# Optimization experiments

Measured on AMD Instinct MI355X. Metric: run time of the kernel, lower is better.

The kernel has to match this reference:

```python
import jax, jax.numpy as jnp
import numpy as np

MAX_W, MIN_W = 120, 24


def setup_inputs() -> dict:
    key = jax.random.key(0)
    ks = jax.random.split(key, 11)
    B, S, D, H = 2, 2048, 1024, 16
    hd = D // H
    s = 1.0 / float(np.sqrt(D))
    return {
        "x": jax.random.normal(ks[0], (B, S, D), jnp.float32),
        "alpha": jnp.float32(0.1),
        "Wq": jax.random.normal(ks[1], (D, D), jnp.float32) * s,
        "bq": jnp.zeros((D,), jnp.float32),
        "Wk": jax.random.normal(ks[2], (D, D), jnp.float32) * s,
        "bk": jnp.zeros((D,), jnp.float32),
        "Wv": jax.random.normal(ks[3], (D, D), jnp.float32) * s,
        "bv": jnp.zeros((D,), jnp.float32),
        "W_o": jax.random.normal(ks[4], (H, hd, hd), jnp.float32),
        "Wfc": jax.random.normal(ks[5], (D, D), jnp.float32) * s,
        "bfc": jnp.zeros((D,), jnp.float32),
    }


def reference(x, alpha, Wq, bq, Wk, bk, Wv, bv, W_o, Wfc, bfc):
    B, S, D = x.shape
    H, hd, _ = W_o.shape
    # --- dynamic window size (step==0 path of the module) ---
    fluct = jnp.abs(x[:, -1] - x[:, -2])            # [B, D]
    a = jax.nn.sigmoid(alpha)
    ewma_prev = fluct[0, 0]                          # step==0: ewma_prev = fluct_step_value
    signal = a * fluct.mean() + (1.0 - a) * ewma_prev
    scale = jax.nn.sigmoid(signal)
    w = jnp.floor(MIN_W + (MAX_W - MIN_W) * scale).astype(jnp.int32)  # int() truncation
    half = w // 2
    # --- projections ---
    q = (x @ Wq + bq).reshape(B, S, H, hd).transpose(0, 2, 1, 3)  # [B,H,S,hd]
    k = (x @ Wk + bk).reshape(B, S, H, hd).transpose(0, 2, 1, 3)
    v = (x @ Wv + bv).reshape(B, S, H, hd).transpose(0, 2, 1, 3)
    inv_sqrt = 1.0 / float(np.sqrt(hd))
    scores = jnp.einsum('bhqd,bhkd->bhqk', q, k) * inv_sqrt       # [B,H,S,S]
    # banded window mask: allowed iff i - w//2 <= j <= i + w//2
    idx = jnp.arange(S)
    band = jnp.abs(idx[:, None] - idx[None, :]) <= half            # [S,S]
    scores = jnp.where(band[None, None], scores, -1e30)
    attn = jax.nn.softmax(scores, axis=-1)
    out = jnp.einsum('bhqk,bhkd->bhqd', attn, v)                   # [B,H,S,hd]
    out = jnp.einsum('bhqd,hdk->bhqk', out, W_o)                   # per-head output matmul
    out = out.transpose(0, 2, 1, 3).reshape(B, S, D)
    return out @ Wfc + bfc
```

## Files before the change

### kernel.cpp

```cpp
#include <hip/hip_runtime.h>
#include <hip/hip_bf16.h>
#include <stdint.h>
#include <stddef.h>

#define S_LEN 2048
#define DMODEL 1024
#define NHEAD 16
#define HDIM 64
#define BATCH 2
#define MROWS (BATCH * S_LEN)
#define QKV_LD 3072

typedef unsigned short u16;
typedef __attribute__((ext_vector_type(8))) short bf16x8;
typedef __attribute__((ext_vector_type(4))) float f32x4;

__device__ inline u16 f32_to_bf16(float f) {
  union { float f; unsigned int u; } v; v.f = f;
  unsigned int u = v.u;
  unsigned int r = (u + 0x7fffu + ((u >> 16) & 1u)) >> 16;
  return (u16)r;
}

__device__ inline void gload16(const u16* g, u16* l) {
  __builtin_amdgcn_global_load_lds(
      (const __attribute__((address_space(1))) unsigned int*)g,
      (__attribute__((address_space(3))) unsigned int*)l, 16, 0, 0);
}

__global__ __launch_bounds__(256) void prep(const float* __restrict__ x, u16* __restrict__ xb,
                                            const float* __restrict__ alpha, int* __restrict__ halfw,
                                            const float* __restrict__ Wq, const float* __restrict__ Wk,
                                            const float* __restrict__ Wv, u16* __restrict__ Wt) {
  __shared__ float lds[32 * 33];
  const int bid = blockIdx.x, tid = threadIdx.x;

  if (bid < 2048) {
    size_t i = ((size_t)bid * 256 + tid) * 8;
    float4 v0 = *(const float4*)(x + i);
    float4 v1 = *(const float4*)(x + i + 4);
    bf16x8 r;
    r[0] = (short)f32_to_bf16(v0.x); r[1] = (short)f32_to_bf16(v0.y);
    r[2] = (short)f32_to_bf16(v0.z); r[3] = (short)f32_to_bf16(v0.w);
    r[4] = (short)f32_to_bf16(v1.x); r[5] = (short)f32_to_bf16(v1.y);
    r[6] = (short)f32_to_bf16(v1.z); r[7] = (short)f32_to_bf16(v1.w);
    *(bf16x8*)(xb + i) = r;
  } else if (bid == 2048) {
    float s = 0.f;
    for (int i = tid; i < BATCH * DMODEL; i += 256) {
      int b = i >> 10, d = i & 1023;
      size_t base = (size_t)b * S_LEN * DMODEL + d;
      float f1 = x[base + (size_t)(S_LEN - 1) * DMODEL];
      float f0 = x[base + (size_t)(S_LEN - 2) * DMODEL];
      s += fabsf(f1 - f0);
    }
#pragma unroll
    for (int m = 32; m >= 1; m >>= 1) s += __shfl_xor(s, m, 64);
    if ((tid & 63) == 0) lds[tid >> 6] = s;
    __syncthreads();
    if (tid == 0) {
      float total = lds[0] + lds[1] + lds[2] + lds[3];
      float mean = total / (float)(BATCH * DMODEL);
      float e1 = x[(size_t)(S_LEN - 1) * DMODEL];
      float e0 = x[(size_t)(S_LEN - 2) * DMODEL];
      float ew = fabsf(e1 - e0);
      float a = 1.f / (1.f + expf(-alpha[0]));
      float sig = a * mean + (1.f - a) * ew;
      float scale = 1.f / (1.f + expf(-sig));
      int wv = (int)floorf(24.f + 96.f * scale);
      *halfw = wv >> 1;
    }
  } else {
    float (*tile)[33] = (float (*)[33])lds;
    const int r = bid - 2049;
    const int z = r >> 10, rem = r & 1023;
    const int k0 = (rem >> 5) * 32, n0 = (rem & 31) * 32;
    const float* W = z == 0 ? Wq : (z == 1 ? Wk : Wv);
    const int tx = tid & 31, ty = tid >> 5;
#pragma unroll
    for (int i = 0; i < 4; ++i)
      tile[ty + i * 8][tx] = W[(size_t)(k0 + ty + i * 8) * DMODEL + n0 + tx];
    __syncthreads();
    u16* o = Wt + (size_t)z * DMODEL * DMODEL;
#pragma unroll
    for (int i = 0; i < 4; ++i)
      o[(size_t)(n0 + ty + i * 8) * DMODEL + k0 + tx] = f32_to_bf16(tile[tx][ty + i * 8]);
  }
}

__global__ __launch_bounds__(128) void build_wc(const float* __restrict__ W_o,
                                                const float* __restrict__ Wfc,
                                                u16* __restrict__ Wc_t) {
  __shared__ float lds[64 * 128];
  int nb = blockIdx.x, h = blockIdx.y, tx = threadIdx.x;
  int n0 = nb * 128;
#pragma unroll
  for (int c = 0; c < 64; ++c)
    lds[c * 128 + tx] = Wfc[(size_t)(h * 64 + c) * DMODEL + n0 + tx];
  __syncthreads();
  float acc[64];
#pragma unroll
  for (int d = 0; d < 64; ++d) acc[d] = 0.f;
  for (int c = 0; c < 64; ++c) {
    float wv = lds[c * 128 + tx];
#pragma unroll
    for (int d = 0; d < 64; ++d)
      acc[d] += W_o[(size_t)(h * 64 + d) * 64 + c] * wv;
  }
  u16 tmp[64];
#pragma unroll
  for (int d = 0; d < 64; ++d) tmp[d] = f32_to_bf16(acc[d]);
  u16* dst = Wc_t + (size_t)(n0 + tx) * DMODEL + h * 64;
#pragma unroll
  for (int q = 0; q < 8; ++q)
    *(bf16x8*)(dst + q * 8) = *(bf16x8*)(tmp + q * 8);
}

__global__ __launch_bounds__(256, 2) void gemm_qkv(
    const u16* __restrict__ A, const u16* __restrict__ Bt,
    const float* __restrict__ bq, const float* __restrict__ bk,
    const float* __restrict__ bv, u16* __restrict__ out) {
  __shared__ __align__(16) u16 smem[2][256 * 64];

  const int tid = threadIdx.x;
  const int l = tid & 63, w = tid >> 6;
  const int wr = w >> 1, wc = w & 1;
  const int lrow = l & 15, lk = l >> 4;

  const int xcd = blockIdx.x & 7;
  const int idx = blockIdx.x >> 3;
  const int bm = idx & 31;
  const int bn = xcd * 3 + (idx >> 5);
  const int rowA0 = bm * 128;
  const int colB0 = bn * 128;

  f32x4 acc[4][4] = {};

  auto stage = [&](int buf, int kt) {
    u16* As = smem[buf];
    u16* Bs = smem[buf] + 128 * 64;
#pragma unroll
    for (int i = 0; i < 4; ++i) {
      int c = i * 256 + tid;
      int row = c >> 3, u = c & 7;
      const u16* g = A + (size_t)(rowA0 + row) * DMODEL + kt + ((u ^ (row & 7)) << 3);
      gload16(g, As + c * 8);
    }
#pragma unroll
    for (int i = 0; i < 4; ++i) {
      int c = i * 256 + tid;
      int row = c >> 3, u = c & 7;
      const u16* g = Bt + (size_t)(colB0 + row) * DMODEL + kt + ((u ^ (row & 7)) << 3);
      gload16(g, Bs + c * 8);
    }
  };

  stage(0, 0);

  int buf = 0;
#pragma unroll 1
  for (int t = 0; t < 16; ++t) {
    __builtin_amdgcn_s_barrier();
    if (t < 15) {
      stage(buf ^ 1, (t + 1) * 64);
      asm volatile("s_waitcnt vmcnt(8)" ::: "memory");
    } else {
      asm volatile("s_waitcnt vmcnt(0)" ::: "memory");
    }
    __builtin_amdgcn_s_barrier();
    asm volatile("" ::: "memory");

    const u16* As = smem[buf];
    const u16* Bs = smem[buf] + 128 * 64;
    __builtin_amdgcn_s_setprio(1);
#pragma unroll
    for (int kk = 0; kk < 2; ++kk) {
      const int swz = ((((kk << 2) + lk) ^ (lrow & 7)) << 3);
      bf16x8 af[4], bg[4];
#pragma unroll
      for (int m = 0; m < 4; ++m)
        af[m] = *(const bf16x8*)(As + (wr * 64 + m * 16 + lrow) * 64 + swz);
#pragma unroll
      for (int n = 0; n < 4; ++n)
        bg[n] = *(const bf16x8*)(Bs + (wc * 64 + n * 16 + lrow) * 64 + swz);
#pragma unroll
      for (int m = 0; m < 4; ++m)
#pragma unroll
        for (int n = 0; n < 4; ++n)
          acc[m][n] = __builtin_amdgcn_mfma_f32_16x16x32_bf16(af[m], bg[n], acc[m][n], 0, 0, 0);
    }
    __builtin_amdgcn_s_setprio(0);
    buf ^= 1;
  }

#pragma unroll
  for (int n = 0; n < 4; ++n) {
    int c = colB0 + wc * 64 + n * 16 + lrow;
    float bias = (c < 1024) ? bq[c] : ((c < 2048) ? bk[c - 1024] : bv[c - 2048]);
    float mult = (c < 1024) ? 0.125f : 1.0f;
#pragma unroll
    for (int m = 0; m < 4; ++m) {
      int r0 = rowA0 + wr * 64 + m * 16 + lk * 4;
#pragma unroll
      for (int j = 0; j < 4; ++j)
        out[(size_t)(r0 + j) * QKV_LD + c] = f32_to_bf16((acc[m][n][j] + bias) * mult);
    }
  }
}

__global__ __launch_bounds__(256, 2) void gemm_fc(const u16* __restrict__ A,
                                                  const u16* __restrict__ Bt,
                                                  const float* __restrict__ bias,
                                                  float* __restrict__ out) {
  __shared__ __align__(16) u16 smem[2][192 * 64];

  const int tid = threadIdx.x;
  const int l = tid & 63, w = tid >> 6;
  const int wr = w >> 1, wc = w & 1;
  const int lrow = l & 15, lk = l >> 4;

  const int bn = blockIdx.x & 7;
  const int bm = blockIdx.x >> 3;
  const int rowA0 = bm * 64, colB0 = bn * 128;

  f32x4 acc[2][4] = {};

  auto stage = [&](int buf, int kt) {
    u16* As = smem[buf];
    u16* Bs = smem[buf] + 64 * 64;
#pragma unroll
    for (int i = 0; i < 2; ++i) {
      int c = i * 256 + tid;
      int row = c >> 3, u = c & 7;
      const u16* g = A + (size_t)(rowA0 + row) * DMODEL + kt + ((u ^ (row & 7)) << 3);
      gload16(g, As + c * 8);
    }
#pragma unroll
    for (int i = 0; i < 4; ++i) {
      int c = i * 256 + tid;
      int row = c >> 3, u = c & 7;
      const u16* g = Bt + (size_t)(colB0 + row) * DMODEL + kt + ((u ^ (row & 7)) << 3);
      gload16(g, Bs + c * 8);
    }
  };

  stage(0, 0);

  int buf = 0;
#pragma unroll 1
  for (int t = 0; t < 16; ++t) {
    __builtin_amdgcn_s_barrier();
    if (t < 15) {
      stage(buf ^ 1, (t + 1) * 64);
      asm volatile("s_waitcnt vmcnt(6)" ::: "memory");
    } else {
      asm volatile("s_waitcnt vmcnt(0)" ::: "memory");
    }
    __builtin_amdgcn_s_barrier();
    asm volatile("" ::: "memory");

    const u16* As = smem[buf];
    const u16* Bs = smem[buf] + 64 * 64;
    __builtin_amdgcn_s_setprio(1);
#pragma unroll
    for (int kk = 0; kk < 2; ++kk) {
      const int swz = ((((kk << 2) + lk) ^ (lrow & 7)) << 3);
      bf16x8 af[2], bg[4];
#pragma unroll
      for (int m = 0; m < 2; ++m)
        af[m] = *(const bf16x8*)(As + (wr * 32 + m * 16 + lrow) * 64 + swz);
#pragma unroll
      for (int n = 0; n < 4; ++n)
        bg[n] = *(const bf16x8*)(Bs + (wc * 64 + n * 16 + lrow) * 64 + swz);
#pragma unroll
      for (int m = 0; m < 2; ++m)
#pragma unroll
        for (int n = 0; n < 4; ++n)
          acc[m][n] = __builtin_amdgcn_mfma_f32_16x16x32_bf16(af[m], bg[n], acc[m][n], 0, 0, 0);
    }
    __builtin_amdgcn_s_setprio(0);
    buf ^= 1;
  }

#pragma unroll
  for (int n = 0; n < 4; ++n) {
    int c = colB0 + wc * 64 + n * 16 + lrow;
    float bv = bias[c];
#pragma unroll
    for (int m = 0; m < 2; ++m) {
      int r0 = rowA0 + wr * 32 + m * 16 + lk * 4;
#pragma unroll
      for (int j = 0; j < 4; ++j)
        out[(size_t)(r0 + j) * DMODEL + c] = acc[m][n][j] + bv;
    }
  }
}

__global__ __launch_bounds__(256) void attn_win(const u16* __restrict__ qkv,
                                                u16* __restrict__ ao,
                                                const int* __restrict__ halfptr) {
  __shared__ __align__(16) u16 KP[12800];
  __shared__ __align__(16) u16 Vt[64 * 200];
  const int tid = threadIdx.x, l = tid & 63, w = tid >> 6;
  const int lrow = l & 15, lk = l >> 4;
  const int q0 = blockIdx.x * 64, k0 = q0 - 64;
  const int h = blockIdx.y, b = blockIdx.z;
  const int halfw = *halfptr;

  const u16* qb = qkv;
  const u16* kb = qkv + 1024;
  const u16* vb = qkv + 2048;

#pragma unroll
  for (int i = 0; i < 6; ++i) {
    int c = i * 256 + tid;
    int row = c >> 3, u = c & 7;
    const u16* g = kb + (ptrdiff_t)((b * S_LEN + k0 + row) * QKV_LD + h * 64 + ((u ^ (row & 7)) << 3));
    gload16(g, KP + c * 8);
  }
  const int qrow = q0 + w * 16 + lrow;
  bf16x8 qf[2];
#pragma unroll
  for (int kk = 0; kk < 2; ++kk)
    qf[kk] = *(const bf16x8*)(qb + (ptrdiff_t)((b * S_LEN + qrow) * QKV_LD + h * 64 + kk * 32 + lk * 8));
  bf16x8 vreg[6];
#pragma unroll
  for (int i = 0; i < 6; ++i) {
    int c = i * 256 + tid;
    int row = c % 192, ch = c / 192;
    vreg[i] = *(const bf16x8*)(vb + (ptrdiff_t)((b * S_LEN + k0 + row) * QKV_LD + h * 64 + ch * 8));
  }

  asm volatile("s_waitcnt vmcnt(0)" ::: "memory");
  __syncthreads();

  f32x4 sc[12];
#pragma unroll
  for (int f = 0; f < 12; ++f) sc[f] = (f32x4){0.f, 0.f, 0.f, 0.f};
#pragma unroll
  for (int kk = 0; kk < 2; ++kk) {
#pragma unroll
    for (int f = 0; f < 12; ++f) {
      bf16x8 kf = *(const bf16x8*)(KP + (f * 16 + lrow) * 64 + ((((kk << 2) + lk) ^ (lrow & 7)) << 3));
      sc[f] = __builtin_amdgcn_mfma_f32_16x16x32_bf16(qf[kk], kf, sc[f], 0, 0, 0);
    }
  }

#pragma unroll
  for (int i = 0; i < 6; ++i) {
    int c = i * 256 + tid;
    int row = c % 192, ch = c / 192;
#pragma unroll
    for (int e = 0; e < 8; ++e)
      Vt[(ch * 8 + e) * 200 + row] = (u16)vreg[i][e];
  }

  float rmax[4] = {-3e38f, -3e38f, -3e38f, -3e38f};
  const int qbase = q0 + w * 16 + lk * 4;
#pragma unroll
  for (int f = 0; f < 12; ++f) {
    int kj = k0 + f * 16 + lrow;
    bool kok = (kj >= 0) && (kj < S_LEN);
#pragma unroll
    for (int j = 0; j < 4; ++j) {
      int qi = qbase + j;
      float v = sc[f][j];
      int dd = qi - kj;
      int ad = dd < 0 ? -dd : dd;
      v = (kok && ad <= halfw) ? v : -1e30f;
      sc[f][j] = v;
      rmax[j] = fmaxf(rmax[j], v);
    }
  }
#pragma unroll
  for (int j = 0; j < 4; ++j) {
    rmax[j] = fmaxf(rmax[j], __shfl_xor(rmax[j], 1, 16));
    rmax[j] = fmaxf(rmax[j], __shfl_xor(rmax[j], 2, 16));
    rmax[j] = fmaxf(rmax[j], __shfl_xor(rmax[j], 4, 16));
    rmax[j] = fmaxf(rmax[j], __shfl_xor(rmax[j], 8, 16));
  }
  float rsum[4] = {0.f, 0.f, 0.f, 0.f};
#pragma unroll
  for (int f = 0; f < 12; ++f)
#pragma unroll
    for (int j = 0; j < 4; ++j) {
      float e = __expf(sc[f][j] - rmax[j]);
      sc[f][j] = e;
      rsum[j] += e;
    }
#pragma unroll
  for (int j = 0; j < 4; ++j) {
    rsum[j] += __shfl_xor(rsum[j], 1, 16);
    rsum[j] += __shfl_xor(rsum[j], 2, 16);
    rsum[j] += __shfl_xor(rsum[j], 4, 16);
    rsum[j] += __shfl_xor(rsum[j], 8, 16);
  }
  float rinv[4];
#pragma unroll
  for (int j = 0; j < 4; ++j) rinv[j] = 1.0f / rsum[j];

  __syncthreads();

  u16* Ps = KP;
#pragma unroll
  for (int f = 0; f < 12; ++f)
#pragma unroll
    for (int j = 0; j < 4; ++j) {
      int prow = w * 16 + lk * 4 + j;
      Ps[prow * 200 + f * 16 + lrow] = f32_to_bf16(sc[f][j] * rinv[j]);
    }
  __syncthreads();

  f32x4 o[4] = {};
#pragma unroll
  for (int jt = 0; jt < 6; ++jt) {
    bf16x8 pa = *(const bf16x8*)(Ps + (w * 16 + lrow) * 200 + jt * 32 + lk * 8);
#pragma unroll
    for (int n = 0; n < 4; ++n) {
      bf16x8 vf = *(const bf16x8*)(Vt + (n * 16 + lrow) * 200 + jt * 32 + lk * 8);
      o[n] = __builtin_amdgcn_mfma_f32_16x16x32_bf16(pa, vf, o[n], 0, 0, 0);
    }
  }
#pragma unroll
  for (int n = 0; n < 4; ++n)
#pragma unroll
    for (int j = 0; j < 4; ++j) {
      int qi = q0 + w * 16 + lk * 4 + j;
      int d = n * 16 + lrow;
      ao[(size_t)(b * S_LEN + qi) * DMODEL + h * 64 + d] = f32_to_bf16(o[n][j]);
    }
}

extern "C" void kernel_launch(void* const* d_in, const int* in_sizes, int n_in,
                              void* d_out, int out_size, void* d_ws, size_t ws_size,
                              hipStream_t stream) {
  (void)in_sizes; (void)n_in; (void)out_size; (void)ws_size;
  const float* x     = (const float*)d_in[0];
  const float* alpha = (const float*)d_in[1];
  const float* Wq    = (const float*)d_in[2];
  const float* bq    = (const float*)d_in[3];
  const float* Wk    = (const float*)d_in[4];
  const float* bk    = (const float*)d_in[5];
  const float* Wv    = (const float*)d_in[6];
  const float* bv    = (const float*)d_in[7];
  const float* W_o   = (const float*)d_in[8];
  const float* Wfc   = (const float*)d_in[9];
  const float* bfc   = (const float*)d_in[10];

  char* ws = (char*)d_ws;
  int* halfw  = (int*)ws;
  u16* xb     = (u16*)(ws + 256);
  u16* Wqkv_t = xb + (size_t)MROWS * DMODEL;
  u16* qkv    = Wqkv_t + (size_t)3 * DMODEL * DMODEL;
  u16* ao     = qkv + (size_t)MROWS * QKV_LD;
  u16* Wc_t   = ao + (size_t)MROWS * DMODEL;

  hipLaunchKernelGGL(prep, dim3(5121), dim3(256), 0, stream,
                     x, xb, alpha, halfw, Wq, Wk, Wv, Wqkv_t);
  hipLaunchKernelGGL(build_wc, dim3(8, 16), dim3(128), 0, stream, W_o, Wfc, Wc_t);
  hipLaunchKernelGGL(gemm_qkv, dim3(768), dim3(256), 0, stream,
                     xb, Wqkv_t, bq, bk, bv, qkv);
  hipLaunchKernelGGL(attn_win, dim3(S_LEN / 64, NHEAD, BATCH), dim3(256), 0, stream,
                     qkv, ao, halfw);
  hipLaunchKernelGGL(gemm_fc, dim3(512), dim3(256), 0, stream,
                     ao, Wc_t, bfc, (float*)d_out);
}
```

Measured before the change: 104.6 us.

## Write V transposed from QKV GEMM, skip masked key tiles, single-buffer GEMMs

The QKV GEMM now writes V directly into a per-batch transposed [D,S] buffer, so the attention kernel can DMA V straight into LDS instead of loading it into registers and transposing with scalar LDS stores. Attention also skips QK MFMAs and softmax work for 16-key fragments wholly outside the current window. Both GEMMs drop double-buffered LDS prefetching in favour of single-buffered load, wait and compute steps, which halves their LDS use and raises occupancy, at the cost of exposing global-load latency. V staging adds clamped out-of-range reads at sequence edges, and those columns are multiplied by zero probabilities.

```diff
diff --git a/kernel.cpp b/kernel.cpp
--- a/kernel.cpp
+++ b/kernel.cpp
@@ -9,10 +9,11 @@
 #define HDIM 64
 #define BATCH 2
 #define MROWS (BATCH * S_LEN)
-#define QKV_LD 3072
+#define QK_LD 2048
 
 typedef unsigned short u16;
 typedef __attribute__((ext_vector_type(8))) short bf16x8;
+typedef __attribute__((ext_vector_type(4))) short bf16x4;
 typedef __attribute__((ext_vector_type(4))) float f32x4;
 
 __device__ inline u16 f32_to_bf16(float f) {
@@ -116,11 +117,11 @@
     *(bf16x8*)(dst + q * 8) = *(bf16x8*)(tmp + q * 8);
 }
 
-__global__ __launch_bounds__(256, 2) void gemm_qkv(
+__global__ __launch_bounds__(256, 3) void gemm_qkv(
     const u16* __restrict__ A, const u16* __restrict__ Bt,
     const float* __restrict__ bq, const float* __restrict__ bk,
-    const float* __restrict__ bv, u16* __restrict__ out) {
-  __shared__ __align__(16) u16 smem[2][256 * 64];
+    const float* __restrict__ bv, u16* __restrict__ out, u16* __restrict__ vt) {
+  __shared__ __align__(16) u16 smem[128 * 64 * 2];
 
   const int tid = threadIdx.x;
   const int l = tid & 63, w = tid >> 6;
@@ -135,10 +136,12 @@
   const int colB0 = bn * 128;
 
   f32x4 acc[4][4] = {};
-
-  auto stage = [&](int buf, int kt) {
-    u16* As = smem[buf];
-    u16* Bs = smem[buf] + 128 * 64;
+  u16* As = smem;
+  u16* Bs = smem + 128 * 64;
+
+#pragma unroll 1
+  for (int t = 0; t < 16; ++t) {
+    const int kt = t * 64;
 #pragma unroll
     for (int i = 0; i < 4; ++i) {
       int c = i * 256 + tid;
@@ -153,26 +156,8 @@
       const u16* g = Bt + (size_t)(colB0 + row) * DMODEL + kt + ((u ^ (row & 7)) << 3);
       gload16(g, Bs + c * 8);
     }
-  };
-
-  stage(0, 0);
-
-  int buf = 0;
-#pragma unroll 1
-  for (int t = 0; t < 16; ++t) {
-    __builtin_amdgcn_s_barrier();
-    if (t < 15) {
-      stage(buf ^ 1, (t + 1) * 64);
-      asm volatile("s_waitcnt vmcnt(8)" ::: "memory");
-    } else {
-      asm volatile("s_waitcnt vmcnt(0)" ::: "memory");
-    }
-    __builtin_amdgcn_s_barrier();
-    asm volatile("" ::: "memory");
-
-    const u16* As = smem[buf];
-    const u16* Bs = smem[buf] + 128 * 64;
-    __builtin_amdgcn_s_setprio(1);
+    asm volatile("s_waitcnt vmcnt(0)");
+    __syncthreads();
 #pragma unroll
     for (int kk = 0; kk < 2; ++kk) {
       const int swz = ((((kk << 2) + lk) ^ (lrow & 7)) << 3);
@@ -189,21 +174,34 @@
         for (int n = 0; n < 4; ++n)
           acc[m][n] = __builtin_amdgcn_mfma_f32_16x16x32_bf16(af[m], bg[n], acc[m][n], 0, 0, 0);
     }
-    __builtin_amdgcn_s_setprio(0);
-    buf ^= 1;
+    __syncthreads();
   }
 
 #pragma unroll
   for (int n = 0; n < 4; ++n) {
     int c = colB0 + wc * 64 + n * 16 + lrow;
-    float bias = (c < 1024) ? bq[c] : ((c < 2048) ? bk[c - 1024] : bv[c - 2048]);
-    float mult = (c < 1024) ? 0.125f : 1.0f;
-#pragma unroll
-    for (int m = 0; m < 4; ++m) {
-      int r0 = rowA0 + wr * 64 + m * 16 + lk * 4;
-#pragma unroll
-      for (int j = 0; j < 4; ++j)
-        out[(size_t)(r0 + j) * QKV_LD + c] = f32_to_bf16((acc[m][n][j] + bias) * mult);
+    if (c < 2048) {
+      float bias = (c < 1024) ? bq[c] : bk[c - 1024];
+      float mult = (c < 1024) ? 0.125f : 1.0f;
+#pragma unroll
+      for (int m = 0; m < 4; ++m) {
+        int r0 = rowA0 + wr * 64 + m * 16 + lk * 4;
+#pragma unroll
+        for (int j = 0; j < 4; ++j)
+          out[(size_t)(r0 + j) * QK_LD + c] = f32_to_bf16((acc[m][n][j] + bias) * mult);
+      }
+    } else {
+      const int dfull = c - 2048;
+      const float bias = bv[dfull];
+#pragma unroll
+      for (int m = 0; m < 4; ++m) {
+        int r0 = rowA0 + wr * 64 + m * 16 + lk * 4;
+        int bb = r0 >> 11, s = r0 & 2047;
+        bf16x4 p;
+#pragma unroll
+        for (int j = 0; j < 4; ++j) p[j] = (short)f32_to_bf16(acc[m][n][j] + bias);
+        *(bf16x4*)(vt + ((size_t)bb << 21) + (size_t)dfull * 2048 + s) = p;
+      }
     }
   }
 }
@@ -212,7 +210,7 @@
                                                   const u16* __restrict__ Bt,
                                                   const float* __restrict__ bias,
                                                   float* __restrict__ out) {
-  __shared__ __align__(16) u16 smem[2][192 * 64];
+  __shared__ __align__(16) u16 smem[(64 + 128) * 64];
 
   const int tid = threadIdx.x;
   const int l = tid & 63, w = tid >> 6;
@@ -224,10 +222,12 @@
   const int rowA0 = bm * 64, colB0 = bn * 128;
 
   f32x4 acc[2][4] = {};
-
-  auto stage = [&](int buf, int kt) {
-    u16* As = smem[buf];
-    u16* Bs = smem[buf] + 64 * 64;
+  u16* As = smem;
+  u16* Bs = smem + 64 * 64;
+
+#pragma unroll 1
+  for (int t = 0; t < 16; ++t) {
+    const int kt = t * 64;
 #pragma unroll
     for (int i = 0; i < 2; ++i) {
       int c = i * 256 + tid;
@@ -242,26 +242,8 @@
       const u16* g = Bt + (size_t)(colB0 + row) * DMODEL + kt + ((u ^ (row & 7)) << 3);
       gload16(g, Bs + c * 8);
     }
-  };
-
-  stage(0, 0);
-
-  int buf = 0;
-#pragma unroll 1
-  for (int t = 0; t < 16; ++t) {
-    __builtin_amdgcn_s_barrier();
-    if (t < 15) {
-      stage(buf ^ 1, (t + 1) * 64);
-      asm volatile("s_waitcnt vmcnt(6)" ::: "memory");
-    } else {
-      asm volatile("s_waitcnt vmcnt(0)" ::: "memory");
-    }
-    __builtin_amdgcn_s_barrier();
-    asm volatile("" ::: "memory");
-
-    const u16* As = smem[buf];
-    const u16* Bs = smem[buf] + 64 * 64;
-    __builtin_amdgcn_s_setprio(1);
+    asm volatile("s_waitcnt vmcnt(0)");
+    __syncthreads();
 #pragma unroll
     for (int kk = 0; kk < 2; ++kk) {
       const int swz = ((((kk << 2) + lk) ^ (lrow & 7)) << 3);
@@ -278,8 +260,7 @@
         for (int n = 0; n < 4; ++n)
           acc[m][n] = __builtin_amdgcn_mfma_f32_16x16x32_bf16(af[m], bg[n], acc[m][n], 0, 0, 0);
     }
-    __builtin_amdgcn_s_setprio(0);
-    buf ^= 1;
+    __syncthreads();
   }
 
 #pragma unroll
@@ -297,42 +278,57 @@
 }
 
 __global__ __launch_bounds__(256) void attn_win(const u16* __restrict__ qkv,
+                                                const u16* __restrict__ vt,
                                                 u16* __restrict__ ao,
                                                 const int* __restrict__ halfptr) {
   __shared__ __align__(16) u16 KP[12800];
-  __shared__ __align__(16) u16 Vt[64 * 200];
+  __shared__ __align__(16) u16 Vs[12800];
   const int tid = threadIdx.x, l = tid & 63, w = tid >> 6;
   const int lrow = l & 15, lk = l >> 4;
   const int q0 = blockIdx.x * 64, k0 = q0 - 64;
   const int h = blockIdx.y, b = blockIdx.z;
   const int halfw = *halfptr;
+  const int f_lo = (64 - halfw) >> 4;
+  const int f_hi = (127 + halfw) >> 4;
 
   const u16* qb = qkv;
   const u16* kb = qkv + 1024;
-  const u16* vb = qkv + 2048;
 
 #pragma unroll
   for (int i = 0; i < 6; ++i) {
     int c = i * 256 + tid;
     int row = c >> 3, u = c & 7;
-    const u16* g = kb + (ptrdiff_t)((b * S_LEN + k0 + row) * QKV_LD + h * 64 + ((u ^ (row & 7)) << 3));
+    const u16* g = kb + (ptrdiff_t)((b * S_LEN + k0 + row) * QK_LD + h * 64 + ((u ^ (row & 7)) << 3));
     gload16(g, KP + c * 8);
   }
   const int qrow = q0 + w * 16 + lrow;
   bf16x8 qf[2];
 #pragma unroll
   for (int kk = 0; kk < 2; ++kk)
-    qf[kk] = *(const bf16x8*)(qb + (ptrdiff_t)((b * S_LEN + qrow) * QKV_LD + h * 64 + kk * 32 + lk * 8));
-  bf16x8 vreg[6];
+    qf[kk] = *(const bf16x8*)(qb + (ptrdiff_t)((b * S_LEN + qrow) * QK_LD + h * 64 + kk * 32 + lk * 8));
 #pragma unroll
   for (int i = 0; i < 6; ++i) {
-    int c = i * 256 + tid;
-    int row = c % 192, ch = c / 192;
-    vreg[i] = *(const bf16x8*)(vb + (ptrdiff_t)((b * S_LEN + k0 + row) * QKV_LD + h * 64 + ch * 8));
-  }
-
-  asm volatile("s_waitcnt vmcnt(0)" ::: "memory");
-  __syncthreads();
+    int o = i * 256 + tid;
+    int d = o / 25, ch = o - d * 25;
+    int kc = k0 + ch * 8;
+    kc = kc < 0 ? 0 : (kc > 2040 ? 2040 : kc);
+    const u16* g = vt + ((size_t)b << 21) + (size_t)(h * 64 + d) * 2048 + kc;
+    gload16(g, Vs + o * 8);
+  }
+  {
+    int o = 1536 + tid;
+    if (o < 1600) {
+      int d = o / 25, ch = o - d * 25;
+      int kc = k0 + ch * 8;
+      kc = kc < 0 ? 0 : (kc > 2040 ? 2040 : kc);
+      const u16* g = vt + ((size_t)b << 21) + (size_t)(h * 64 + d) * 2048 + kc;
+      gload16(g, Vs + o * 8);
+    }
+  }
+
+  asm volatile("s_waitcnt vmcnt(6)" ::: "memory");
+  __builtin_amdgcn_s_barrier();
+  asm volatile("" ::: "memory");
 
   f32x4 sc[12];
 #pragma unroll
@@ -341,24 +337,18 @@
   for (int kk = 0; kk < 2; ++kk) {
 #pragma unroll
     for (int f = 0; f < 12; ++f) {
-      bf16x8 kf = *(const bf16x8*)(KP + (f * 16 + lrow) * 64 + ((((kk << 2) + lk) ^ (lrow & 7)) << 3));
-      sc[f] = __builtin_amdgcn_mfma_f32_16x16x32_bf16(qf[kk], kf, sc[f], 0, 0, 0);
-    }
-  }
-
-#pragma unroll
-  for (int i = 0; i < 6; ++i) {
-    int c = i * 256 + tid;
-    int row = c % 192, ch = c / 192;
-#pragma unroll
-    for (int e = 0; e < 8; ++e)
-      Vt[(ch * 8 + e) * 200 + row] = (u16)vreg[i][e];
+      if (f >= f_lo && f <= f_hi) {
+        bf16x8 kf = *(const bf16x8*)(KP + (f * 16 + lrow) * 64 + ((((kk << 2) + lk) ^ (lrow & 7)) << 3));
+        sc[f] = __builtin_amdgcn_mfma_f32_16x16x32_bf16(qf[kk], kf, sc[f], 0, 0, 0);
+      }
+    }
   }
 
   float rmax[4] = {-3e38f, -3e38f, -3e38f, -3e38f};
   const int qbase = q0 + w * 16 + lk * 4;
 #pragma unroll
   for (int f = 0; f < 12; ++f) {
+    if (f < f_lo || f > f_hi) continue;
     int kj = k0 + f * 16 + lrow;
     bool kok = (kj >= 0) && (kj < S_LEN);
 #pragma unroll
@@ -381,13 +371,15 @@
   }
   float rsum[4] = {0.f, 0.f, 0.f, 0.f};
 #pragma unroll
-  for (int f = 0; f < 12; ++f)
+  for (int f = 0; f < 12; ++f) {
+    if (f < f_lo || f > f_hi) { sc[f] = (f32x4){0.f, 0.f, 0.f, 0.f}; continue; }
 #pragma unroll
     for (int j = 0; j < 4; ++j) {
       float e = __expf(sc[f][j] - rmax[j]);
       sc[f][j] = e;
       rsum[j] += e;
     }
+  }
 #pragma unroll
   for (int j = 0; j < 4; ++j) {
     rsum[j] += __shfl_xor(rsum[j], 1, 16);
@@ -399,7 +391,8 @@
 #pragma unroll
   for (int j = 0; j < 4; ++j) rinv[j] = 1.0f / rsum[j];
 
-  __syncthreads();
+  __builtin_amdgcn_s_barrier();
+  asm volatile("" ::: "memory");
 
   u16* Ps = KP;
 #pragma unroll
@@ -409,7 +402,9 @@
       int prow = w * 16 + lk * 4 + j;
       Ps[prow * 200 + f * 16 + lrow] = f32_to_bf16(sc[f][j] * rinv[j]);
     }
-  __syncthreads();
+  asm volatile("s_waitcnt lgkmcnt(0) vmcnt(0)" ::: "memory");
+  __builtin_amdgcn_s_barrier();
+  asm volatile("" ::: "memory");
 
   f32x4 o[4] = {};
 #pragma unroll
@@ -417,7 +412,7 @@
     bf16x8 pa = *(const bf16x8*)(Ps + (w * 16 + lrow) * 200 + jt * 32 + lk * 8);
 #pragma unroll
     for (int n = 0; n < 4; ++n) {
-      bf16x8 vf = *(const bf16x8*)(Vt + (n * 16 + lrow) * 200 + jt * 32 + lk * 8);
+      bf16x8 vf = *(const bf16x8*)(Vs + (n * 16 + lrow) * 200 + jt * 32 + lk * 8);
       o[n] = __builtin_amdgcn_mfma_f32_16x16x32_bf16(pa, vf, o[n], 0, 0, 0);
     }
   }
@@ -452,16 +447,17 @@
   u16* xb     = (u16*)(ws + 256);
   u16* Wqkv_t = xb + (size_t)MROWS * DMODEL;
   u16* qkv    = Wqkv_t + (size_t)3 * DMODEL * DMODEL;
-  u16* ao     = qkv + (size_t)MROWS * QKV_LD;
+  u16* vt     = qkv + (size_t)MROWS * QK_LD;
+  u16* ao     = vt + (size_t)BATCH * DMODEL * S_LEN;
   u16* Wc_t   = ao + (size_t)MROWS * DMODEL;
 
   hipLaunchKernelGGL(prep, dim3(5121), dim3(256), 0, stream,
                      x, xb, alpha, halfw, Wq, Wk, Wv, Wqkv_t);
   hipLaunchKernelGGL(build_wc, dim3(8, 16), dim3(128), 0, stream, W_o, Wfc, Wc_t);
   hipLaunchKernelGGL(gemm_qkv, dim3(768), dim3(256), 0, stream,
-                     xb, Wqkv_t, bq, bk, bv, qkv);
+                     xb, Wqkv_t, bq, bk, bv, qkv, vt);
   hipLaunchKernelGGL(attn_win, dim3(S_LEN / 64, NHEAD, BATCH), dim3(256), 0, stream,
-                     qkv, ao, halfw);
+                     qkv, vt, ao, halfw);
   hipLaunchKernelGGL(gemm_fc, dim3(512), dim3(256), 0, stream,
                      ao, Wc_t, bfc, (float*)d_out);
 }
```

Result: faster. 100.7 us (-3.7%).
